# Kernel tuning notes

Hardware: AMD Instinct MI355X
Metric: run time of the kernel (lower is better)

## Reference

```python
import jax, jax.numpy as jnp
import numpy as np

ALPHA = 0.2  # leaky relu slope
NEG_INF = -1.0e12


def _gat(x, adj, W, a):
    # x: [N, Fin], W: [Fin, Fout], a: [2*Fout, 1]
    h = x @ W                                  # [N, Fout]
    Fout = W.shape[1]
    # additive attention: e_ij = leakyrelu(h_i . a[:Fout] + h_j . a[Fout:])
    f1 = h @ a[:Fout, 0]                       # [N]
    f2 = h @ a[Fout:, 0]                       # [N]
    e = jax.nn.leaky_relu(f1[:, None] + f2[None, :], ALPHA)  # [N, N]
    att = jnp.where(adj > 0, e, NEG_INF)
    att = jax.nn.softmax(att, axis=1)          # dropout=0 -> identity
    return jax.nn.elu(att @ h + h)             # [N, Fout]


def setup_inputs() -> dict:
    key = jax.random.key(0)
    k = jax.random.split(key, 6)
    N, NFEAT, NHID, NNEXT = 8192, 256, 128, 1024
    x = jax.random.normal(k[0], (N, NFEAT), dtype=jnp.float32)
    adj = (jax.random.uniform(k[1], (N, N)) > 0.9).astype(jnp.float32)
    # xavier-uniform-ish init
    def xav(kk, shape):
        lim = np.sqrt(6.0 / (shape[0] + shape[1])) * 1.414
        return jax.random.uniform(kk, shape, minval=-lim, maxval=lim, dtype=jnp.float32)
    W_embed = xav(k[2], (NFEAT, NHID))
    a_embed = xav(k[3], (2 * NHID, 1))
    W_assign = xav(k[4], (NFEAT, NNEXT))
    a_assign = xav(k[5], (2 * NNEXT, 1))
    return {"x": x, "adj": adj, "W_embed": W_embed, "a_embed": a_embed,
            "W_assign": W_assign, "a_assign": a_assign}


def reference(x, adj, W_embed, a_embed, W_assign, a_assign):
    z_l = _gat(x, adj, W_embed, a_embed)          # [N, nhid]
    assign = _gat(x, adj, W_assign, a_assign)     # [N, nnext]
    s_l = jax.nn.softmax(assign, axis=-1)         # [N, nnext]
    xnext = s_l.T @ z_l                            # [nnext, nhid]
    anext = s_l.T @ adj @ s_l                      # [nnext, nnext]
    return xnext, anext, s_l
```

## Files before the change

### kernel.cpp

```cpp
#include <hip/hip_runtime.h>
#include <hip/hip_bf16.h>


#define DI __device__ __forceinline__

typedef __attribute__((ext_vector_type(8))) short short8;
typedef __attribute__((ext_vector_type(4))) float f32x4;

static DI float bf2f(short s) {
    union { unsigned u; float f; } c;
    c.u = ((unsigned)(unsigned short)s) << 16;
    return c.f;
}
static DI short f2bf(float f) {
    union { float f; unsigned u; } c; c.f = f;
    unsigned r = (c.u + 0x7FFFu + ((c.u >> 16) & 1u)) >> 16;
    return (short)(unsigned short)r;
}
static DI short f2bf_tr(float f) {
    union { float f; unsigned u; } c; c.f = f;
    return (short)(unsigned short)(c.u >> 16);
}
template <int F32>
static DI short8 ld8(const void* base, size_t off) {
    if (F32 == 0) return *(const short8*)((const short*)base + off);
    const float* p = (const float*)base + off;
    f32x4 a = *(const f32x4*)p;
    f32x4 b = *(const f32x4*)(p + 4);
    short8 v;
    #pragma unroll
    for (int e = 0; e < 4; e++) { v[e] = f2bf(a[e]); v[4 + e] = f2bf(b[e]); }
    return v;
}
static DI float wred_sum(float v) {
    #pragma unroll
    for (int o = 32; o > 0; o >>= 1) v += __shfl_down(v, o, 64);
    return v;
}
static DI float wred_max(float v) {
    #pragma unroll
    for (int o = 32; o > 0; o >>= 1) v = fmaxf(v, __shfl_down(v, o, 64));
    return v;
}
static DI int sfun(int r) { return (r ^ (r >> 3)) & 7; }
static DI int swzk(int k, int r) {
    return (k & ~63) | ((((k >> 3) & 7) ^ sfun(r)) << 3) | (k & 7);
}
static DI unsigned pack2(short lo, short hi) {
    return ((unsigned)(unsigned short)lo) | (((unsigned)(unsigned short)hi) << 16);
}
static DI void gload16(const void* g, void* l) {
    __builtin_amdgcn_global_load_lds(
        (const __attribute__((address_space(1))) unsigned int*)g,
        (__attribute__((address_space(3))) unsigned int*)l, 16, 0, 0);
}

template <int EPI, int SWZX>
__launch_bounds__(256)
__global__ void gemm_lds(const short* __restrict__ A, const short* __restrict__ Bt,
                         void* __restrict__ C, int ldc, int kcount) {
    __shared__ short As0[128][64], Bs0[128][64];
    __shared__ short As1[128][64], Bs1[128][64];
    int bx = blockIdx.x, by = blockIdx.y;
    if (SWZX) {
        int lid = blockIdx.x + blockIdx.y * 8;
        int c = lid & 7, s = lid >> 3;
        by = c * 8 + (s >> 3);
        bx = s & 7;
    }
    const int tid  = threadIdx.x;
    const int lane = tid & 63;
    const int w    = tid >> 6;
    const int wr   = w >> 1, wc = w & 1;
    const int i0   = by * 128;
    const int n0   = bx * 128;
    const int k0   = blockIdx.z * kcount;

    const int srow = w * 32 + (lane >> 3);
    const short* gA = A  + (size_t)(i0 + srow) * 8192 + k0 + (lane & 7) * 8;
    const short* gB = Bt + (size_t)(n0 + srow) * 8192 + k0 + (lane & 7) * 8;

    f32x4 acc[4][4];
    #pragma unroll
    for (int m = 0; m < 4; m++)
        #pragma unroll
        for (int n = 0; n < 4; n++) acc[m][n] = (f32x4){0.f, 0.f, 0.f, 0.f};

#define STAGE_TILE(ts, Ab, Bb)                                                  \
    do {                                                                        \
        _Pragma("unroll")                                                       \
        for (int j = 0; j < 4; j++) {                                           \
            gload16(gA + (size_t)(ts) * 64 + (size_t)j * 8 * 8192,              \
                    &Ab[w * 32 + j * 8][0]);                                    \
            gload16(gB + (size_t)(ts) * 64 + (size_t)j * 8 * 8192,              \
                    &Bb[w * 32 + j * 8][0]);                                    \
        }                                                                       \
    } while (0)

#define COMPUTE_TILE(Ab, Bb)                                                    \
    do {                                                                        \
        _Pragma("unroll")                                                       \
        for (int kk = 0; kk < 2; kk++) {                                        \
            short8 af[4], bq[4];                                                \
            _Pragma("unroll")                                                   \
            for (int m = 0; m < 4; m++) {                                       \
                int ar = wr * 64 + m * 16 + (lane & 15);                        \
                af[m] = *(const short8*)&Ab[ar]                                 \
                            [swzk(kk * 32 + (lane >> 4) * 8, ar)];              \
            }                                                                   \
            _Pragma("unroll")                                                   \
            for (int n = 0; n < 4; n++) {                                       \
                int br = wc * 64 + n * 16 + (lane & 15);                        \
                bq[n] = *(const short8*)&Bb[br]                                 \
                            [swzk(kk * 32 + (lane >> 4) * 8, br)];              \
            }                                                                   \
            _Pragma("unroll")                                                   \
            for (int m = 0; m < 4; m++)                                         \
                _Pragma("unroll")                                               \
                for (int n = 0; n < 4; n++)                                     \
                    acc[m][n] = __builtin_amdgcn_mfma_f32_16x16x32_bf16(        \
                        af[m], bq[n], acc[m][n], 0, 0, 0);                      \
        }                                                                       \
    } while (0)

    const int nt = kcount >> 6;
    STAGE_TILE(0, As0, Bs0);
    for (int t = 0; t < nt; t += 2) {
        __syncthreads();
        STAGE_TILE(t + 1, As1, Bs1);
        COMPUTE_TILE(As0, Bs0);
        __syncthreads();
        if (t + 2 < nt) STAGE_TILE(t + 2, As0, Bs0);
        COMPUTE_TILE(As1, Bs1);
    }
#undef STAGE_TILE

    #pragma unroll
    for (int m = 0; m < 4; m++) {
        #pragma unroll
        for (int n = 0; n < 4; n++) {
            int row0 = i0 + wr * 64 + m * 16 + ((lane >> 4) << 2);
            int col  = n0 + wc * 64 + n * 16 + (lane & 15);
            if (EPI == 1) {
                unsigned long long pk = 0;
                #pragma unroll
                for (int r = 0; r < 4; r++)
                    pk |= (unsigned long long)(unsigned short)f2bf(acc[m][n][r])
                          << (16 * r);
                *(unsigned long long*)((short*)C + (size_t)col * 8192 +
                                       swzk(row0, col)) = pk;
            } else {
                #pragma unroll
                for (int r = 0; r < 4; r++) {
                    float v = acc[m][n][r];
                    if (EPI == 0) ((float*)C)[(size_t)(row0 + r) * ldc + col] = v;
                    else atomicAdd(&((float*)C)[(size_t)(row0 + r) * ldc + col], v);
                }
            }
        }
    }
#undef COMPUTE_TILE
}

template <int EPI>
__launch_bounds__(256)
__global__ void gemm_gen(const short* __restrict__ Ab, const short* __restrict__ Bt,
                         float* __restrict__ C, int ldc, int kcount,
                         const float* __restrict__ E1, const float* __restrict__ F1,
                         const float* __restrict__ E2, const float* __restrict__ F2) {
    __shared__ short As0[128][64], Bs0[128][64];
    __shared__ short As1[128][64], Bs1[128][64];
    const int tid  = threadIdx.x;
    const int lane = tid & 63;
    const int w    = tid >> 6;
    const int wr   = w >> 1, wc = w & 1;
    const int i0   = blockIdx.y * 128;
    const int n0   = blockIdx.x * 128;
    const int k0   = blockIdx.z * kcount;

    const int srow = w * 32 + (lane >> 3);
    const short* gB = Bt + (size_t)(n0 + srow) * 8192 + k0 + (lane & 7) * 8;

    f32x4 acc[4][4];
    #pragma unroll
    for (int m = 0; m < 4; m++)
        #pragma unroll
        for (int n = 0; n < 4; n++) acc[m][n] = (f32x4){0.f, 0.f, 0.f, 0.f};

    short8 avr[4];

#define G_ALOAD(ts)                                                             \
    do {                                                                        \
        _Pragma("unroll")                                                       \
        for (int it = 0; it < 4; it++) {                                        \
            int idx = it * 256 + tid;                                           \
            int r = idx >> 3, kb = idx & 7;                                     \
            avr[it] = *(const short8*)(Ab + (size_t)(i0 + r) * 8192 + k0 +      \
                                       (size_t)(ts) * 64 + kb * 8);             \
        }                                                                       \
    } while (0)

#define G_BLOAD(ts, Bb)                                                         \
    do {                                                                        \
        _Pragma("unroll")                                                       \
        for (int j = 0; j < 4; j++)                                             \
            gload16(gB + (size_t)(ts) * 64 + (size_t)j * 8 * 8192,              \
                    &Bb[w * 32 + j * 8][0]);                                    \
    } while (0)

#define G_WSTAGE(ts, As_)                                                       \
    do {                                                                        \
        _Pragma("unroll")                                                       \
        for (int it = 0; it < 4; it++) {                                        \
            int idx = it * 256 + tid;                                           \
            int r = idx >> 3, kb = idx & 7;                                     \
            int kl = k0 + (ts) * 64 + ((kb ^ sfun(r)) << 3);                    \
            float e1r = E1[i0 + r], f1r = F1[i0 + r];                           \
            f32x4 e2a = *(const f32x4*)(E2 + kl);                               \
            f32x4 e2b = *(const f32x4*)(E2 + kl + 4);                           \
            f32x4 f2a = *(const f32x4*)(F2 + kl);                               \
            f32x4 f2b = *(const f32x4*)(F2 + kl + 4);                           \
            short8 av = avr[it], p;                                             \
            _Pragma("unroll")                                                   \
            for (int e = 0; e < 8; e++) {                                       \
                float ev = e < 4 ? e2a[e] : e2b[e - 4];                         \
                float fv = e < 4 ? f2a[e] : f2b[e - 4];                         \
                float wg = fmaxf(e1r * ev, f1r * fv);                           \
                p[e] = ((unsigned short)av[e]) ? f2bf(wg) : (short)0;           \
            }                                                                   \
            *(short8*)&As_[r][kb * 8] = p;                                      \
        }                                                                       \
    } while (0)

#define G_COMPUTE(Ab_, Bb_)                                                     \
    do {                                                                        \
        _Pragma("unroll")                                                       \
        for (int kk = 0; kk < 2; kk++) {                                        \
            short8 af[4], bq[4];                                                \
            _Pragma("unroll")                                                   \
            for (int m = 0; m < 4; m++) {                                       \
                int ar = wr * 64 + m * 16 + (lane & 15);                        \
                af[m] = *(const short8*)&Ab_[ar]                                \
                            [swzk(kk * 32 + (lane >> 4) * 8, ar)];              \
            }                                                                   \
            _Pragma("unroll")                                                   \
            for (int n = 0; n < 4; n++) {                                       \
                int br = wc * 64 + n * 16 + (lane & 15);                        \
                bq[n] = *(const short8*)&Bb_[br]                                \
                            [swzk(kk * 32 + (lane >> 4) * 8, br)];              \
            }                                                                   \
            _Pragma("unroll")                                                   \
            for (int m = 0; m < 4; m++)                                         \
                _Pragma("unroll")                                               \
                for (int n = 0; n < 4; n++)                                     \
                    acc[m][n] = __builtin_amdgcn_mfma_f32_16x16x32_bf16(        \
                        af[m], bq[n], acc[m][n], 0, 0, 0);                      \
        }                                                                       \
    } while (0)

    const int nt = kcount >> 6;
    G_ALOAD(0);
    G_BLOAD(0, Bs0);
    for (int t = 0; t < nt; t += 2) {
        G_WSTAGE(t, As0);
        __syncthreads();
        G_ALOAD(t + 1);
        G_BLOAD(t + 1, Bs1);
        G_COMPUTE(As0, Bs0);
        G_WSTAGE(t + 1, As1);
        __syncthreads();
        if (t + 2 < nt) { G_ALOAD(t + 2); G_BLOAD(t + 2, Bs0); }
        G_COMPUTE(As1, Bs1);
    }
#undef G_ALOAD
#undef G_BLOAD
#undef G_WSTAGE
#undef G_COMPUTE

    #pragma unroll
    for (int m = 0; m < 4; m++) {
        #pragma unroll
        for (int n = 0; n < 4; n++) {
            int row0 = i0 + wr * 64 + m * 16 + ((lane >> 4) << 2);
            int col  = n0 + wc * 64 + n * 16 + (lane & 15);
            #pragma unroll
            for (int r = 0; r < 4; r++)
                atomicAdd(&C[(size_t)(row0 + r) * ldc + col], acc[m][n][r]);
        }
    }
}

template <int SWZX>
__launch_bounds__(256)
__global__ void gemm_xw_k(const float* __restrict__ A, const float* __restrict__ B,
                          short* __restrict__ C, short* __restrict__ Ct, int ldn) {
    __shared__ short As[128][64];
    __shared__ short Bs[128][64];
    int bx = blockIdx.x, by = blockIdx.y;
    if (SWZX) {
        int lid = blockIdx.x + blockIdx.y * 8;
        int c = lid & 7, s = lid >> 3;
        by = c * 8 + (s >> 3);
        bx = s & 7;
    }
    const int tid  = threadIdx.x;
    const int lane = tid & 63;
    const int w    = tid >> 6;
    const int wr   = w >> 1, wc = w & 1;
    const int i0   = by * 128;
    const int n0   = bx * 128;

    f32x4 acc[4][4];
    #pragma unroll
    for (int m = 0; m < 4; m++)
        #pragma unroll
        for (int n = 0; n < 4; n++) acc[m][n] = (f32x4){0.f, 0.f, 0.f, 0.f};

    for (int ks = 0; ks < 256; ks += 64) {
        __syncthreads();
        #pragma unroll
        for (int it = 0; it < 4; it++) {
            int idx = it * 256 + tid;
            int cg = idx & 7, r = idx >> 3;
            *(short8*)&As[r][swzk(cg * 8, r)] =
                ld8<1>(A, (size_t)(i0 + r) * 256 + ks + cg * 8);
        }
        #pragma unroll
        for (int it = 0; it < 2; it++) {
            int idx = it * 256 + tid;
            int ng = idx & 15, kp = idx >> 4;
            int k = 2 * kp;
            short8 r0 = ld8<1>(B, (size_t)(ks + k) * ldn + n0 + ng * 8);
            short8 r1 = ld8<1>(B, (size_t)(ks + k + 1) * ldn + n0 + ng * 8);
            #pragma unroll
            for (int j = 0; j < 8; j++) {
                int row = ng * 8 + j;
                *(unsigned*)&Bs[row][swzk(k, row)] = pack2(r0[j], r1[j]);
            }
        }
        __syncthreads();
        #pragma unroll
        for (int kk = 0; kk < 2; kk++) {
            short8 af[4], bq[4];
            #pragma unroll
            for (int m = 0; m < 4; m++) {
                int ar = wr * 64 + m * 16 + (lane & 15);
                af[m] = *(const short8*)&As[ar][swzk(kk * 32 + (lane >> 4) * 8, ar)];
            }
            #pragma unroll
            for (int n = 0; n < 4; n++) {
                int br = wc * 64 + n * 16 + (lane & 15);
                bq[n] = *(const short8*)&Bs[br][swzk(kk * 32 + (lane >> 4) * 8, br)];
            }
            #pragma unroll
            for (int m = 0; m < 4; m++)
                #pragma unroll
                for (int n = 0; n < 4; n++)
                    acc[m][n] = __builtin_amdgcn_mfma_f32_16x16x32_bf16(
                        af[m], bq[n], acc[m][n], 0, 0, 0);
        }
    }
    #pragma unroll
    for (int m = 0; m < 4; m++) {
        #pragma unroll
        for (int n = 0; n < 4; n++) {
            int row0 = i0 + wr * 64 + m * 16 + ((lane >> 4) << 2);
            int col  = n0 + wc * 64 + n * 16 + (lane & 15);
            unsigned long long pk = 0;
            #pragma unroll
            for (int r = 0; r < 4; r++) {
                short b = f2bf(acc[m][n][r]);
                C[(size_t)(row0 + r) * ldn + col] = b;
                pk |= (unsigned long long)(unsigned short)b << (16 * r);
            }
            *(unsigned long long*)(Ct + (size_t)col * 8192 + swzk(row0, col)) = pk;
        }
    }
}

__launch_bounds__(256)
__global__ void compute_f_k(const short* __restrict__ h1, const short* __restrict__ h2,
                            const float* __restrict__ ae, const float* __restrict__ aa,
                            float* __restrict__ f11, float* __restrict__ f21,
                            float* __restrict__ f12, float* __restrict__ f22) {
    int row = blockIdx.x, t = threadIdx.x;
    float s11 = 0.f, s21 = 0.f, s12 = 0.f, s22 = 0.f;
    if (t < 128) {
        float hv = bf2f(h1[(size_t)row * 128 + t]);
        s11 = hv * ae[t];
        s21 = hv * ae[128 + t];
    }
    #pragma unroll
    for (int q = 0; q < 4; q++) {
        int f = t + q * 256;
        float hv = bf2f(h2[(size_t)row * 1024 + f]);
        s12 += hv * aa[f];
        s22 += hv * aa[1024 + f];
    }
    __shared__ float red[4][4];
    s11 = wred_sum(s11); s21 = wred_sum(s21);
    s12 = wred_sum(s12); s22 = wred_sum(s22);
    int w = t >> 6;
    if ((t & 63) == 0) { red[0][w] = s11; red[1][w] = s21; red[2][w] = s12; red[3][w] = s22; }
    __syncthreads();
    if (t == 0) {
        f11[row] = red[0][0] + red[0][1] + red[0][2] + red[0][3];
        f21[row] = red[1][0] + red[1][1] + red[1][2] + red[1][3];
        f12[row] = red[2][0] + red[2][1] + red[2][2] + red[2][3];
        f22[row] = red[3][0] + red[3][1] + red[3][2] + red[3][3];
    }
}

__launch_bounds__(256)
__global__ void evec_k(const float* __restrict__ f11, const float* __restrict__ f21,
                       const float* __restrict__ f12, const float* __restrict__ f22,
                       float* __restrict__ E11, float* __restrict__ F11,
                       float* __restrict__ E21, float* __restrict__ F21,
                       float* __restrict__ E12, float* __restrict__ F12,
                       float* __restrict__ E22, float* __restrict__ F22) {
    int i = blockIdx.x * 256 + threadIdx.x;
    if (i >= 8192) return;
    float a = f11[i], b = f21[i], c = f12[i], d = f22[i];
    E11[i] = __expf(a); F11[i] = __expf(0.2f * a);
    E21[i] = __expf(b); F21[i] = __expf(0.2f * b);
    E12[i] = __expf(c); F12[i] = __expf(0.2f * c);
    E22[i] = __expf(d); F22[i] = __expf(0.2f * d);
}

__launch_bounds__(256)
__global__ void prepass_k(const float* __restrict__ adj,
                          const float* __restrict__ E11, const float* __restrict__ F11,
                          const float* __restrict__ E21, const float* __restrict__ F21,
                          const float* __restrict__ E12, const float* __restrict__ F12,
                          const float* __restrict__ E22, const float* __restrict__ F22,
                          float* __restrict__ den1, float* __restrict__ den2,
                          short* __restrict__ adjb, short* __restrict__ P2b) {
    int row = blockIdx.x, t = threadIdx.x;
    float e1r = E11[row], f1r = F11[row];
    float e2r = E12[row], f2r = F12[row];
    float d1 = 0.f, d2 = 0.f;
    const float* arow = adj + (size_t)row * 8192;
    #pragma unroll
    for (int it = 0; it < 4; it++) {
        int jb = (it * 256 + t) * 8;
        size_t wo = (size_t)row * 8192 + swzk(jb, row);
        f32x4 a0 = *(const f32x4*)(arow + jb), a1 = *(const f32x4*)(arow + jb + 4);
        f32x4 eA0 = *(const f32x4*)(E21 + jb), eA1 = *(const f32x4*)(E21 + jb + 4);
        f32x4 fA0 = *(const f32x4*)(F21 + jb), fA1 = *(const f32x4*)(F21 + jb + 4);
        f32x4 eB0 = *(const f32x4*)(E22 + jb), eB1 = *(const f32x4*)(E22 + jb + 4);
        f32x4 fB0 = *(const f32x4*)(F22 + jb), fB1 = *(const f32x4*)(F22 + jb + 4);
        short8 ab, p2v;
        #pragma unroll
        for (int e = 0; e < 8; e++) {
            float av = e < 4 ? a0[e] : a1[e - 4];
            float eA = e < 4 ? eA0[e] : eA1[e - 4];
            float fA = e < 4 ? fA0[e] : fA1[e - 4];
            float eB = e < 4 ? eB0[e] : eB1[e - 4];
            float fB = e < 4 ? fB0[e] : fB1[e - 4];
            float x1 = fmaxf(e1r * eA, f1r * fA);
            float x2 = fmaxf(e2r * eB, f2r * fB);
            float p1 = av > 0.f ? x1 : 0.f;
            float p2 = av > 0.f ? x2 : 0.f;
            d1 += p1; d2 += p2;
            ab[e] = f2bf_tr(av); p2v[e] = f2bf(p2);
        }
        *(short8*)(adjb + wo) = ab;
        *(short8*)(P2b  + wo) = p2v;
    }
    __shared__ float r1[4], r2[4];
    d1 = wred_sum(d1); d2 = wred_sum(d2);
    if ((t & 63) == 0) { r1[t >> 6] = d1; r2[t >> 6] = d2; }
    __syncthreads();
    if (t == 0) {
        den1[row] = r1[0] + r1[1] + r1[2] + r1[3];
        den2[row] = r2[0] + r2[1] + r2[2] + r2[3];
    }
}

__launch_bounds__(256)
__global__ void epi_gat1t_k(const float* __restrict__ Y1, const float* __restrict__ den1,
                            const short* __restrict__ h1, short* __restrict__ zlt) {
    __shared__ short ts[128][65];
    int tr = blockIdx.x * 64;
    int t = threadIdx.x;
    #pragma unroll
    for (int it = 0; it < 4; it++) {
        int idx = it * 256 + t;
        int r = idx >> 4, cb = idx & 15;
        int row = tr + r;
        float d = den1[row]; d = d > 0.f ? d : 1.f;
        const float* yp = Y1 + (size_t)row * 128 + cb * 8;
        f32x4 y0 = *(const f32x4*)yp, y1 = *(const f32x4*)(yp + 4);
        short8 hv = *(const short8*)(h1 + (size_t)row * 128 + cb * 8);
        #pragma unroll
        for (int e = 0; e < 8; e++) {
            float z = (e < 4 ? y0[e] : y1[e - 4]) / d + bf2f(hv[e]);
            z = z > 0.f ? z : (__expf(z) - 1.f);
            ts[cb * 8 + e][r] = f2bf(z);
        }
    }
    __syncthreads();
    #pragma unroll
    for (int it = 0; it < 4; it++) {
        int idx = it * 256 + t;
        int c = idx >> 3, rb = idx & 7;
        short8 v = *(const short8*)&ts[c][rb * 8];
        *(short8*)(zlt + (size_t)c * 8192 + tr + ((rb ^ sfun(c)) << 3)) = v;
    }
}

__launch_bounds__(256)
__global__ void episoft_k(const float* __restrict__ Y2, const float* __restrict__ den2,
                          const short* __restrict__ h2, float* __restrict__ slo,
                          short* __restrict__ slb) {
    int row = blockIdx.x, t = threadIdx.x;
    float d = den2[row];
    d = d > 0.f ? d : 1.f;
    float v[4], mx = -1e30f;
    #pragma unroll
    for (int q = 0; q < 4; q++) {
        int j = t + q * 256;
        float a = Y2[(size_t)row * 1024 + j] / d + bf2f(h2[(size_t)row * 1024 + j]);
        a = a > 0.f ? a : (__expf(a) - 1.f);
        v[q] = a;
        mx = fmaxf(mx, a);
    }
    __shared__ float sred[4];
    __shared__ float sbc;
    mx = wred_max(mx);
    if ((t & 63) == 0) sred[t >> 6] = mx;
    __syncthreads();
    if (t == 0) sbc = fmaxf(fmaxf(sred[0], sred[1]), fmaxf(sred[2], sred[3]));
    __syncthreads();
    mx = sbc;
    float s = 0.f;
    #pragma unroll
    for (int q = 0; q < 4; q++) { v[q] = __expf(v[q] - mx); s += v[q]; }
    s = wred_sum(s);
    if ((t & 63) == 0) sred[t >> 6] = s;
    __syncthreads();
    if (t == 0) sbc = sred[0] + sred[1] + sred[2] + sred[3];
    __syncthreads();
    float inv = 1.f / sbc;
    #pragma unroll
    for (int q = 0; q < 4; q++) {
        float sv = v[q] * inv;
        slo[(size_t)row * 1024 + t + q * 256] = sv;
        slb[(size_t)row * 1024 + t + q * 256] = f2bf(sv);
    }
}

template <int F32IN>
__launch_bounds__(256)
__global__ void transpose_swz_k(const void* __restrict__ in, short* __restrict__ out,
                                int R, int C) {
    __shared__ short ts[64][72];
    int tc = blockIdx.x * 64;
    int tr = blockIdx.y * 64;
    int t = threadIdx.x;
    #pragma unroll
    for (int h = 0; h < 2; h++) {
        int r = (t >> 3) + h * 32, c = (t & 7) * 8;
        *(short8*)&ts[r][c] = ld8<F32IN>(in, (size_t)(tr + r) * C + tc + c);
    }
    __syncthreads();
    #pragma unroll
    for (int h = 0; h < 2; h++) {
        int n = t >> 2, blk = (t & 3) + h * 4;
        short8 v;
        #pragma unroll
        for (int e = 0; e < 8; e++) v[e] = ts[blk * 8 + e][n];
        *(short8*)(out + (size_t)(tc + n) * R + tr + ((blk ^ sfun(tc + n)) << 3)) = v;
    }
}

extern "C" void kernel_launch(void* const* d_in, const int* in_sizes, int n_in,
                              void* d_out, int out_size, void* d_ws, size_t ws_size,
                              hipStream_t stream) {
    const float* x   = (const float*)d_in[0];
    const float* adj = (const float*)d_in[1];
    const float* We  = (const float*)d_in[2];
    const float* ae  = (const float*)d_in[3];
    const float* Wa  = (const float*)d_in[4];
    const float* aa  = (const float*)d_in[5];
    float* out = (float*)d_out;

    char* w = (char*)d_ws;
    short* h1b = (short*)(w);
    short* h2b = (short*)(w + (2u   << 20));
    float* f11 = (float*)(w + (18u  << 20));
    float* f21 = f11 + 8192;  float* f12 = f21 + 8192; float* f22 = f12 + 8192;
    float* den1 = f22 + 8192; float* den2 = den1 + 8192;
    float* E11 = den2 + 8192; float* F11 = E11 + 8192;
    float* E21 = F11 + 8192;  float* F21 = E21 + 8192;
    float* E12 = F21 + 8192;  float* F12 = E12 + 8192;
    float* E22 = F12 + 8192;  float* F22 = E22 + 8192;
    float* Y1f = (float*)(w + (21u << 20));
    float* Y2f = (float*)(w + (25u << 20));
    short* slb = (short*)(w + (57u << 20));
    short* h1t = (short*)(w + (73u << 20));
    short* h2t = (short*)(w + (75u << 20));
    short* slt = (short*)(w + (91u << 20));
    short* zlt = (short*)(w + (107u << 20));
    short* tT  = (short*)(w + (109u << 20));
    short* adjb = (short*)(w + (128u << 20));
    short* P2b  = (short*)(w + (256u << 20));

    float* xo  = out;
    float* ao  = out + 131072;
    float* slo = out + 131072 + 1048576;

    hipMemsetAsync(out, 0, (size_t)(131072 + 1048576) * 4, stream);
    hipMemsetAsync(Y1f, 0, (size_t)8192 * 128 * 4, stream);

    gemm_xw_k<0><<<dim3(1, 64), 256, 0, stream>>>(x, We, h1b, h1t, 128);
    gemm_xw_k<1><<<dim3(8, 64), 256, 0, stream>>>(x, Wa, h2b, h2t, 1024);
    compute_f_k<<<dim3(8192), 256, 0, stream>>>(h1b, h2b, ae, aa, f11, f21, f12, f22);
    evec_k<<<dim3(32), 256, 0, stream>>>(f11, f21, f12, f22,
        E11, F11, E21, F21, E12, F12, E22, F22);
    prepass_k<<<dim3(8192), 256, 0, stream>>>(adj,
        E11, F11, E21, F21, E12, F12, E22, F22, den1, den2, adjb, P2b);

    gemm_gen<3><<<dim3(1, 64, 8), 256, 0, stream>>>(
        adjb, h1t, Y1f, 128, 1024, E11, F11, E21, F21);
    epi_gat1t_k<<<dim3(128), 256, 0, stream>>>(Y1f, den1, h1b, zlt);

    gemm_lds<0, 1><<<dim3(8, 64, 1), 256, 0, stream>>>(P2b, h2t, Y2f, 1024, 8192);
    episoft_k<<<dim3(8192), 256, 0, stream>>>(Y2f, den2, h2b, slo, slb);
    transpose_swz_k<0><<<dim3(16, 128), 256, 0, stream>>>(slb, slt, 8192, 1024);

    gemm_lds<1, 1><<<dim3(8, 64, 1), 256, 0, stream>>>(adjb, slt, tT, 0, 8192);

    gemm_lds<3, 0><<<dim3(8, 8, 8), 256, 0, stream>>>(slt, tT, ao, 1024, 1024);
    gemm_lds<3, 0><<<dim3(1, 8, 32), 256, 0, stream>>>(slt, zlt, xo, 128, 256);
}
```

Measured before the change: 723.4 us.

## Derive adjacency mask from P2 weights, dropping separate bf16 adjacency buffer

Stops the prepass from writing a bf16 copy of the adjacency matrix and instead reconstructs the 0/1 mask from the nonzero pattern of the masked attention weights inside a generating GEMM. The first attention GEMM and the adj·S GEMM both read P2b, removing a large write and one distinct matrix stream. A block-index swizzle and a bf16 transposed epilogue are added to the generating GEMM. This relies on every attention weight for an edge being nonzero after bf16 rounding.

```diff
diff --git a/kernel.cpp b/kernel.cpp
--- a/kernel.cpp
+++ b/kernel.cpp
@@ -16,10 +16,6 @@
     union { float f; unsigned u; } c; c.f = f;
     unsigned r = (c.u + 0x7FFFu + ((c.u >> 16) & 1u)) >> 16;
     return (short)(unsigned short)r;
-}
-static DI short f2bf_tr(float f) {
-    union { float f; unsigned u; } c; c.f = f;
-    return (short)(unsigned short)(c.u >> 16);
 }
 template <int F32>
 static DI short8 ld8(const void* base, size_t off) {
@@ -162,20 +158,27 @@
 #undef COMPUTE_TILE
 }
 
-template <int EPI>
+template <int EPI, int GEN, int SWZX>
 __launch_bounds__(256)
 __global__ void gemm_gen(const short* __restrict__ Ab, const short* __restrict__ Bt,
-                         float* __restrict__ C, int ldc, int kcount,
+                         void* __restrict__ C, int ldc, int kcount,
                          const float* __restrict__ E1, const float* __restrict__ F1,
                          const float* __restrict__ E2, const float* __restrict__ F2) {
     __shared__ short As0[128][64], Bs0[128][64];
     __shared__ short As1[128][64], Bs1[128][64];
+    int bx = blockIdx.x, by = blockIdx.y;
+    if (SWZX) {
+        int lid = blockIdx.x + blockIdx.y * 8;
+        int c = lid & 7, s = lid >> 3;
+        by = c * 8 + (s >> 3);
+        bx = s & 7;
+    }
     const int tid  = threadIdx.x;
     const int lane = tid & 63;
     const int w    = tid >> 6;
     const int wr   = w >> 1, wc = w & 1;
-    const int i0   = blockIdx.y * 128;
-    const int n0   = blockIdx.x * 128;
+    const int i0   = by * 128;
+    const int n0   = bx * 128;
     const int k0   = blockIdx.z * kcount;
 
     const int srow = w * 32 + (lane >> 3);
@@ -214,19 +217,25 @@
         for (int it = 0; it < 4; it++) {                                        \
             int idx = it * 256 + tid;                                           \
             int r = idx >> 3, kb = idx & 7;                                     \
-            int kl = k0 + (ts) * 64 + ((kb ^ sfun(r)) << 3);                    \
-            float e1r = E1[i0 + r], f1r = F1[i0 + r];                           \
-            f32x4 e2a = *(const f32x4*)(E2 + kl);                               \
-            f32x4 e2b = *(const f32x4*)(E2 + kl + 4);                           \
-            f32x4 f2a = *(const f32x4*)(F2 + kl);                               \
-            f32x4 f2b = *(const f32x4*)(F2 + kl + 4);                           \
             short8 av = avr[it], p;                                             \
-            _Pragma("unroll")                                                   \
-            for (int e = 0; e < 8; e++) {                                       \
-                float ev = e < 4 ? e2a[e] : e2b[e - 4];                         \
-                float fv = e < 4 ? f2a[e] : f2b[e - 4];                         \
-                float wg = fmaxf(e1r * ev, f1r * fv);                           \
-                p[e] = ((unsigned short)av[e]) ? f2bf(wg) : (short)0;           \
+            if (GEN == 1) {                                                     \
+                _Pragma("unroll")                                               \
+                for (int e = 0; e < 8; e++)                                     \
+                    p[e] = ((unsigned short)av[e]) ? (short)0x3F80 : (short)0;  \
+            } else {                                                            \
+                int kl = k0 + (ts) * 64 + ((kb ^ sfun(r)) << 3);                \
+                float e1r = E1[i0 + r], f1r = F1[i0 + r];                       \
+                f32x4 e2a = *(const f32x4*)(E2 + kl);                           \
+                f32x4 e2b = *(const f32x4*)(E2 + kl + 4);                       \
+                f32x4 f2a = *(const f32x4*)(F2 + kl);                           \
+                f32x4 f2b = *(const f32x4*)(F2 + kl + 4);                       \
+                _Pragma("unroll")                                               \
+                for (int e = 0; e < 8; e++) {                                   \
+                    float ev = e < 4 ? e2a[e] : e2b[e - 4];                     \
+                    float fv = e < 4 ? f2a[e] : f2b[e - 4];                     \
+                    float wg = fmaxf(e1r * ev, f1r * fv);                       \
+                    p[e] = ((unsigned short)av[e]) ? f2bf(wg) : (short)0;       \
+                }                                                               \
             }                                                                   \
             *(short8*)&As_[r][kb * 8] = p;                                      \
         }                                                                       \
@@ -283,9 +292,20 @@
         for (int n = 0; n < 4; n++) {
             int row0 = i0 + wr * 64 + m * 16 + ((lane >> 4) << 2);
             int col  = n0 + wc * 64 + n * 16 + (lane & 15);
-            #pragma unroll
-            for (int r = 0; r < 4; r++)
-                atomicAdd(&C[(size_t)(row0 + r) * ldc + col], acc[m][n][r]);
+            if (EPI == 1) {
+                unsigned long long pk = 0;
+                #pragma unroll
+                for (int r = 0; r < 4; r++)
+                    pk |= (unsigned long long)(unsigned short)f2bf(acc[m][n][r])
+                          << (16 * r);
+                *(unsigned long long*)((short*)C + (size_t)col * 8192 +
+                                       swzk(row0, col)) = pk;
+            } else {
+                #pragma unroll
+                for (int r = 0; r < 4; r++)
+                    atomicAdd(&((float*)C)[(size_t)(row0 + r) * ldc + col],
+                              acc[m][n][r]);
+            }
         }
     }
 }
@@ -434,7 +454,7 @@
                           const float* __restrict__ E12, const float* __restrict__ F12,
                           const float* __restrict__ E22, const float* __restrict__ F22,
                           float* __restrict__ den1, float* __restrict__ den2,
-                          short* __restrict__ adjb, short* __restrict__ P2b) {
+                          short* __restrict__ P2b) {
     int row = blockIdx.x, t = threadIdx.x;
     float e1r = E11[row], f1r = F11[row];
     float e2r = E12[row], f2r = F12[row];
@@ -449,7 +469,7 @@
         f32x4 fA0 = *(const f32x4*)(F21 + jb), fA1 = *(const f32x4*)(F21 + jb + 4);
         f32x4 eB0 = *(const f32x4*)(E22 + jb), eB1 = *(const f32x4*)(E22 + jb + 4);
         f32x4 fB0 = *(const f32x4*)(F22 + jb), fB1 = *(const f32x4*)(F22 + jb + 4);
-        short8 ab, p2v;
+        short8 p2v;
         #pragma unroll
         for (int e = 0; e < 8; e++) {
             float av = e < 4 ? a0[e] : a1[e - 4];
@@ -462,10 +482,9 @@
             float p1 = av > 0.f ? x1 : 0.f;
             float p2 = av > 0.f ? x2 : 0.f;
             d1 += p1; d2 += p2;
-            ab[e] = f2bf_tr(av); p2v[e] = f2bf(p2);
-        }
-        *(short8*)(adjb + wo) = ab;
-        *(short8*)(P2b  + wo) = p2v;
+            p2v[e] = f2bf(p2);
+        }
+        *(short8*)(P2b + wo) = p2v;
     }
     __shared__ float r1[4], r2[4];
     d1 = wred_sum(d1); d2 = wred_sum(d2);
@@ -603,8 +622,7 @@
     short* slt = (short*)(w + (91u << 20));
     short* zlt = (short*)(w + (107u << 20));
     short* tT  = (short*)(w + (109u << 20));
-    short* adjb = (short*)(w + (128u << 20));
-    short* P2b  = (short*)(w + (256u << 20));
+    short* P2b = (short*)(w + (128u << 20));
 
     float* xo  = out;
     float* ao  = out + 131072;
@@ -619,17 +637,18 @@
     evec_k<<<dim3(32), 256, 0, stream>>>(f11, f21, f12, f22,
         E11, F11, E21, F21, E12, F12, E22, F22);
     prepass_k<<<dim3(8192), 256, 0, stream>>>(adj,
-        E11, F11, E21, F21, E12, F12, E22, F22, den1, den2, adjb, P2b);
-
-    gemm_gen<3><<<dim3(1, 64, 8), 256, 0, stream>>>(
-        adjb, h1t, Y1f, 128, 1024, E11, F11, E21, F21);
+        E11, F11, E21, F21, E12, F12, E22, F22, den1, den2, P2b);
+
+    gemm_gen<3, 0, 0><<<dim3(1, 64, 8), 256, 0, stream>>>(
+        P2b, h1t, Y1f, 128, 1024, E11, F11, E21, F21);
     epi_gat1t_k<<<dim3(128), 256, 0, stream>>>(Y1f, den1, h1b, zlt);
 
     gemm_lds<0, 1><<<dim3(8, 64, 1), 256, 0, stream>>>(P2b, h2t, Y2f, 1024, 8192);
     episoft_k<<<dim3(8192), 256, 0, stream>>>(Y2f, den2, h2b, slo, slb);
     transpose_swz_k<0><<<dim3(16, 128), 256, 0, stream>>>(slb, slt, 8192, 1024);
 
-    gemm_lds<1, 1><<<dim3(8, 64, 1), 256, 0, stream>>>(adjb, slt, tT, 0, 8192);
+    gemm_gen<1, 1, 1><<<dim3(8, 64, 1), 256, 0, stream>>>(
+        P2b, slt, tT, 0, 8192, nullptr, nullptr, nullptr, nullptr);
 
     gemm_lds<3, 0><<<dim3(8, 8, 8), 256, 0, stream>>>(slt, tT, ao, 1024, 1024);
     gemm_lds<3, 0><<<dim3(1, 8, 32), 256, 0, stream>>>(slt, zlt, xo, 128, 256);
```

New measurement: 721.2 us. About the same (-0.3%).
